# Kernel tuning notes

Measured on AMD Instinct MI355X. Metric: run time of the kernel, lower is better.

## Reference

```python
import jax, jax.numpy as jnp
import numpy as np

PATCH = 16  # patch_size

def _patchify(images, p=PATCH):
    # images: [B, H, W] -> patches: [B, N, p*p] in raster order
    B, H, W = images.shape
    x = images.reshape(B, H // p, p, W // p, p)
    x = x.transpose(0, 1, 3, 2, 4)  # [B, H/p, W/p, p, p]
    return x.reshape(B, (H // p) * (W // p), p * p)

def setup_inputs() -> dict:
    key = jax.random.key(0)
    k1, k2 = jax.random.split(key)
    images = jax.random.normal(k1, (64, 256, 256), dtype=jnp.float32)
    vocab = jax.random.normal(k2, (4096, 256), dtype=jnp.float32)  # [V, patch^2]
    return {"images": images, "vocab": vocab}

def reference(images, vocab):
    # forward_patches: patchify (raster ordering -> identity permutation)
    patches = _patchify(images)  # [B, N, D]
    # forward_tokens: torch.cdist + argmin. argmin of Euclidean distance
    # equals argmin of squared distance; expand ||x-v||^2 to avoid the
    # explicit [B, N, V, D] difference tensor.
    v2 = jnp.sum(vocab * vocab, axis=-1)                      # [V]
    xv = jnp.einsum('bnd,vd->bnv', patches, vocab)            # [B, N, V]
    x2 = jnp.sum(patches * patches, axis=-1, keepdims=True)   # [B, N, 1]
    d2 = x2 - 2.0 * xv + v2                                   # [B, N, V]
    tokens = jnp.argmin(d2, axis=-1)                          # [B, N] int
    return patches, tokens
```

## Files before the change

### kernel.cpp

```cpp
#include <hip/hip_runtime.h>
#include <math.h>

#define PS      16
#define D       256
#define V       4096
#define M       16384
#define NSPLIT  64
#define PAIR_CAP 1048576
#define QMARGIN 130

typedef _Float16 half8 __attribute__((ext_vector_type(8)));
typedef _Float16 half4 __attribute__((ext_vector_type(4)));
typedef float    f32x4 __attribute__((ext_vector_type(4)));

__device__ __forceinline__ void gload_lds16(const void* g, void* l) {
  __builtin_amdgcn_global_load_lds(
      (const __attribute__((address_space(1))) unsigned int*)g,
      (__attribute__((address_space(3))) unsigned int*)l, 16, 0, 0);
}


__global__ __launch_bounds__(256) void prep_kernel(
    const float* __restrict__ img, const float* __restrict__ vocab,
    float* __restrict__ outp, _Float16* __restrict__ Ah2,
    _Float16* __restrict__ Vh2, float* __restrict__ v2,
    int* __restrict__ paircount) {
  if (blockIdx.x < 4096) {
    if (blockIdx.x == 0 && threadIdx.x == 0) *paircount = 0;
    const int t  = blockIdx.x * 256 + threadIdx.x;
    const int o4 = t << 2;
    const int m   = o4 >> 8;
    const int d   = o4 & 255;
    const int b   = m >> 8;
    const int n   = m & 255;
    const int py = n >> 4, px = n & 15, i = d >> 4, j = d & 15;
    const float4 v = *(const float4*)(img + (b << 16) + ((py * PS + i) << 8) + px * PS + j);
    *(float4*)(outp + o4) = v;
    half4 h = { (_Float16)v.x, (_Float16)v.y, (_Float16)v.z, (_Float16)v.w };
    const int fa = (m >> 6) * 16384 + (d >> 5) * 2048 + ((m >> 4) & 3) * 512 +
                   ((d >> 3) & 3) * 128 + (m & 15) * 8 + (d & 7);
    *(half4*)(Ah2 + fa) = h;
  } else {
    const int gtid = (blockIdx.x - 4096) * 256 + threadIdx.x;
    const int c    = gtid >> 6;
    const int lane = gtid & 63;
    const int d0   = lane << 2;
    const float4 v = *(const float4*)(vocab + (size_t)c * D + d0);
    half4 h = { (_Float16)v.x, (_Float16)v.y, (_Float16)v.z, (_Float16)v.w };
    const int fv = (c >> 8) * 65536 + (d0 >> 5) * 8192 + ((c >> 4) & 15) * 512 +
                   ((d0 >> 3) & 3) * 128 + (c & 15) * 8 + (d0 & 7);
    *(half4*)(Vh2 + fv) = h;
    float s = v.x * v.x + v.y * v.y + v.z * v.z + v.w * v.w;
    #pragma unroll
    for (int off = 32; off > 0; off >>= 1) s += __shfl_down(s, off);
    if (lane == 0) v2[c] = s;
  }
}

__global__ __launch_bounds__(512, 6) void gemm_score_kernel(
    const _Float16* __restrict__ Ah2,
    const _Float16* __restrict__ Vh2,
    const float* __restrict__ v2,
    unsigned* __restrict__ pk1, unsigned* __restrict__ pk2) {
  __shared__ __align__(16) _Float16 Af[8 * 64 * 32];

  const int tid  = threadIdx.x;
  const int lane = tid & 63;
  const int wid  = tid >> 6;
  const int sp     = blockIdx.x;
  const int rowblk = blockIdx.y;
  const int row0 = rowblk * 64;
  const int c0w  = sp * 256 + wid * 32;

  {
    const _Float16* src = Ah2 + (size_t)rowblk * 16384 + wid * 2048 + lane * 8;
    _Float16* dst = Af + wid * 2048;
    #pragma unroll
    for (int t = 0; t < 4; ++t)
      gload_lds16(src + t * 512, dst + t * 512);
  }
  __syncthreads();

  const int cl = lane & 15;
  const int q  = lane >> 4;
  const _Float16* Ak = Af + q * 128 + cl * 8;
  const _Float16* Bk = Vh2 + sp * 65536 + wid * 1024 +
                       q * 128 + cl * 8;

  f32x4 acc[2][4];
  #pragma unroll
  for (int i = 0; i < 2; ++i)
    #pragma unroll
    for (int j = 0; j < 4; ++j) acc[i][j] = (f32x4){0.f, 0.f, 0.f, 0.f};

  half8 av0[2], av1[2], bp[4];
#define LAV(B, OFF) do {                                            \
    B[0] = *(const half8*)(Bk + (OFF));                             \
    B[1] = *(const half8*)(Bk + (OFF) + 512);                       \
  } while (0)
#define LBP(OFF) do {                                               \
    bp[0] = *(const half8*)(Ak + (OFF));                            \
    bp[1] = *(const half8*)(Ak + (OFF) + 512);                      \
    bp[2] = *(const half8*)(Ak + (OFF) + 1024);                     \
    bp[3] = *(const half8*)(Ak + (OFF) + 1536);                     \
  } while (0)
#define MMC(AV) do {                                                \
    __builtin_amdgcn_s_setprio(1);                                  \
    acc[0][0] = __builtin_amdgcn_mfma_f32_16x16x32_f16(AV[0], bp[0], acc[0][0], 0, 0, 0); \
    acc[0][1] = __builtin_amdgcn_mfma_f32_16x16x32_f16(AV[0], bp[1], acc[0][1], 0, 0, 0); \
    acc[0][2] = __builtin_amdgcn_mfma_f32_16x16x32_f16(AV[0], bp[2], acc[0][2], 0, 0, 0); \
    acc[0][3] = __builtin_amdgcn_mfma_f32_16x16x32_f16(AV[0], bp[3], acc[0][3], 0, 0, 0); \
    acc[1][0] = __builtin_amdgcn_mfma_f32_16x16x32_f16(AV[1], bp[0], acc[1][0], 0, 0, 0); \
    acc[1][1] = __builtin_amdgcn_mfma_f32_16x16x32_f16(AV[1], bp[1], acc[1][1], 0, 0, 0); \
    acc[1][2] = __builtin_amdgcn_mfma_f32_16x16x32_f16(AV[1], bp[2], acc[1][2], 0, 0, 0); \
    acc[1][3] = __builtin_amdgcn_mfma_f32_16x16x32_f16(AV[1], bp[3], acc[1][3], 0, 0, 0); \
    __builtin_amdgcn_s_setprio(0);                                  \
  } while (0)

  LAV(av0, 0);
  #pragma unroll 1
  for (int kt2 = 0; kt2 < 3; ++kt2) {
    LAV(av1, 8192);
    LBP(0);
    MMC(av0);
    LAV(av0, 16384);
    LBP(2048);
    MMC(av1);
    Bk += 16384; Ak += 4096;
  }
  LAV(av1, 8192);
  LBP(0);
  MMC(av0);
  LBP(2048);
  MMC(av1);
#undef LAV
#undef LBP
#undef MMC

  float Cv[8];
  #pragma unroll
  for (int i = 0; i < 2; ++i) {
    const float4 vq = *(const float4*)(v2 + c0w + i * 16 + q * 4);
    #pragma unroll
    for (int r = 0; r < 4; ++r) Cv[i * 4 + r] = fmaf(vq[r], 512.0f, 524288.0f);
  }
  unsigned wk1[4], wk2[4];
  #pragma unroll
  for (int j = 0; j < 4; ++j) {
    unsigned K1 = 0xFFFFFFFFu, K2 = 0xFFFFFFFFu;
    #pragma unroll
    for (int i = 0; i < 2; ++i)
      #pragma unroll
      for (int r = 0; r < 4; ++r) {
        const unsigned key =
            ((unsigned)fmaf(-1024.0f, acc[i][j][r], Cv[i * 4 + r]) << 12) |
            (unsigned)(c0w + i * 16 + q * 4 + r);
        K2 = min(K2, max(K1, key));
        K1 = min(K1, key);
      }
    #pragma unroll
    for (int mask = 16; mask <= 32; mask <<= 1) {
      const unsigned o1 = (unsigned)__shfl_xor((int)K1, mask);
      const unsigned o2 = (unsigned)__shfl_xor((int)K2, mask);
      K2 = min(min(K2, o2), max(K1, o1));
      K1 = min(K1, o1);
    }
    wk1[j] = K1; wk2[j] = K2;
  }
  __syncthreads();
  unsigned* scr = (unsigned*)Af;
  if (q == 0) {
    #pragma unroll
    for (int j = 0; j < 4; ++j) {
      const int idx = (wid >> 1) * 256 + (wid & 1) * 128 + (j * 16 + cl) * 2;
      scr[idx] = wk1[j]; scr[idx + 1] = wk2[j];
    }
  }
  __syncthreads();
  if (tid < 256) {
    const int pair = tid >> 6, row = tid & 63;
    const unsigned a1k = scr[pair * 256 + row * 2], a2k = scr[pair * 256 + row * 2 + 1];
    const unsigned b1k = scr[pair * 256 + 128 + row * 2], b2k = scr[pair * 256 + 128 + row * 2 + 1];
    const unsigned K2 = min(min(a2k, b2k), max(a1k, b1k));
    const unsigned K1 = min(a1k, b1k);
    const int grp = sp * 4 + pair;
    pk1[(size_t)grp * M + row0 + row] = K1;
    pk2[(size_t)grp * M + row0 + row] = K2;
  }
}

__global__ __launch_bounds__(256) void reduce_gather_kernel(
    const unsigned* __restrict__ pk1, const unsigned* __restrict__ pk2,
    float* __restrict__ tok, unsigned long long* __restrict__ minkey,
    unsigned* __restrict__ pairs, int* __restrict__ paircount) {
  __shared__ unsigned r1[4][64], r2[4][64];
  const int tid = threadIdx.x;
  const int mo  = tid & 63;
  const int wid = tid >> 6;
  const int m = blockIdx.x * 64 + mo;
  unsigned K1 = 0xFFFFFFFFu, K2 = 0xFFFFFFFFu;
  for (int s = wid * 16; s < wid * 16 + 16; ++s) {
    const unsigned b1 = pk1[(size_t)s * M + m];
    const unsigned b2 = pk2[(size_t)s * M + m];
    K2 = min(min(K2, b2), max(K1, b1));
    K1 = min(K1, b1);
  }
  r1[wid][mo] = K1; r2[wid][mo] = K2;
  __syncthreads();
  if (tid < 64) {
    K1 = 0xFFFFFFFFu; K2 = 0xFFFFFFFFu;
    #pragma unroll
    for (int w = 0; w < 4; ++w) {
      const unsigned b1 = r1[w][mo], b2 = r2[w][mo];
      K2 = min(min(K2, b2), max(K1, b1));
      K1 = min(K1, b1);
    }
    tok[m] = (float)(K1 & 4095u);
    minkey[m] = 0xFFFFFFFFFFFFFFFFull;
    if ((int)(K2 >> 12) - (int)(K1 >> 12) <= QMARGIN) {
      const int th = (int)(K1 >> 12) + QMARGIN;
      int cnt = 0;
      for (int s = 0; s < NSPLIT; ++s) {
        const unsigned b1 = pk1[(size_t)s * M + m];
        const unsigned b2 = pk2[(size_t)s * M + m];
        cnt += ((int)(b2 >> 12) <= th) ? 64
             : (((int)(b1 >> 12) <= th) ? 1 : 0);
      }
      int base = atomicAdd(paircount, cnt);
      if (base + cnt <= PAIR_CAP) {
        const unsigned mh = (unsigned)m << 12;
        for (int s = 0; s < NSPLIT; ++s) {
          const unsigned b1 = pk1[(size_t)s * M + m];
          const unsigned b2 = pk2[(size_t)s * M + m];
          if ((int)(b2 >> 12) <= th) {
            for (int r = 0; r < 64; ++r) pairs[base + r] = mh | (unsigned)(s * 64 + r);
            base += 64;
          } else if ((int)(b1 >> 12) <= th) {
            pairs[base++] = mh | (b1 & 4095u);
          }
        }
      }
    }
  }
}

__global__ __launch_bounds__(256) void refine_score(
    const float* __restrict__ patches, const float* __restrict__ vocab,
    const unsigned* __restrict__ pairs, const int* __restrict__ paircount,
    unsigned long long* __restrict__ minkey) {
  const int lane = threadIdx.x & 63;
  const int gw = (blockIdx.x * 256 + threadIdx.x) >> 6;
  const int nw = (gridDim.x * 256) >> 6;
  int np = *paircount;
  if (np > PAIR_CAP) np = PAIR_CAP;
  for (int i = gw; i < np; i += nw) {
    const unsigned pr = pairs[i];
    const int m = pr >> 12, row = pr & 4095;
    const float4 pv = *(const float4*)(patches + (size_t)m * D + (lane << 2));
    const float4 vv = *(const float4*)(vocab + (size_t)row * D + (lane << 2));
    double acc = 0.0, df;
    df = (double)pv.x - (double)vv.x; acc = fma(df, df, acc);
    df = (double)pv.y - (double)vv.y; acc = fma(df, df, acc);
    df = (double)pv.z - (double)vv.z; acc = fma(df, df, acc);
    df = (double)pv.w - (double)vv.w; acc = fma(df, df, acc);
    #pragma unroll
    for (int off = 32; off > 0; off >>= 1) acc += __shfl_down(acc, off);
    if (lane == 0) {
      const unsigned long long key =
          ((unsigned long long)__double_as_longlong(acc) & ~0xFFFull) | (unsigned)row;
      atomicMin(&minkey[m], key);
    }
  }
}

__global__ __launch_bounds__(256) void refine_final(
    const unsigned* __restrict__ pairs, const int* __restrict__ paircount,
    const unsigned long long* __restrict__ minkey, float* __restrict__ tok) {
  int np = *paircount;
  if (np > PAIR_CAP) np = PAIR_CAP;
  for (int i = blockIdx.x * 256 + threadIdx.x; i < np; i += gridDim.x * 256) {
    const int m = pairs[i] >> 12;
    tok[m] = (float)(unsigned)(minkey[m] & 4095ull);
  }
}

extern "C" void kernel_launch(void* const* d_in, const int* in_sizes, int n_in,
                              void* d_out, int out_size, void* d_ws, size_t ws_size,
                              hipStream_t stream) {
  const float* images = (const float*)d_in[0];
  const float* vocab  = (const float*)d_in[1];
  float* out     = (float*)d_out;
  float* patches = out;
  float* tokens  = out + (size_t)M * D;

  char* ws = (char*)d_ws;
  _Float16* Ah2      = (_Float16*)(ws);
  _Float16* Vh2      = (_Float16*)(ws + 8388608);
  float*    v2       = (float*)   (ws + 10485760);
  unsigned* pk1      = (unsigned*)(ws + 10502144);
  unsigned* pk2      = (unsigned*)(ws + 14696448);
  unsigned long long* minkey = (unsigned long long*)(ws + 18890752);
  int*      paircount= (int*)     (ws + 19021824);
  unsigned* pairs    = (unsigned*)(ws + 19021888);

  prep_kernel<<<4096 + 1024, 256, 0, stream>>>(images, vocab, patches, Ah2,
                                               Vh2, v2, paircount);
  gemm_score_kernel<<<dim3(V / 256, M / 64), 512, 0, stream>>>(Ah2, Vh2, v2, pk1, pk2);
  reduce_gather_kernel<<<M / 64, 256, 0, stream>>>(pk1, pk2, tokens, minkey,
                                                   pairs, paircount);
  refine_score<<<512, 256, 0, stream>>>(patches, vocab, pairs, paircount, minkey);
  refine_final<<<64, 256, 0, stream>>>(pairs, paircount, minkey, tokens);
}
```

Baseline: 151.0 us.

## Switch GEMM to 32x32x16 MFMA with matching fragment layouts

Replaces the 16x16x32 MFMA tiling with 32x32x16 MFMA instructions, issuing four larger MFMAs per step instead of eight. The prep kernel writes A and V fp16 in new fragment-friendly layouts to match. The epilogue top-2 reduction is reworked for the new accumulator layout, which needs one cross-half shuffle instead of two. The refine_score grid is also enlarged from 512 to 2048 blocks. The larger MFMA is meant to raise matrix-core throughput and cut per-tile instruction overhead, at the cost of layout changes that must stay consistent across kernels.

```diff
diff --git a/kernel.cpp b/kernel.cpp
--- a/kernel.cpp
+++ b/kernel.cpp
@@ -11,7 +11,7 @@
 
 typedef _Float16 half8 __attribute__((ext_vector_type(8)));
 typedef _Float16 half4 __attribute__((ext_vector_type(4)));
-typedef float    f32x4 __attribute__((ext_vector_type(4)));
+typedef float    f32x16 __attribute__((ext_vector_type(16)));
 
 __device__ __forceinline__ void gload_lds16(const void* g, void* l) {
   __builtin_amdgcn_global_load_lds(
@@ -37,8 +37,8 @@
     const float4 v = *(const float4*)(img + (b << 16) + ((py * PS + i) << 8) + px * PS + j);
     *(float4*)(outp + o4) = v;
     half4 h = { (_Float16)v.x, (_Float16)v.y, (_Float16)v.z, (_Float16)v.w };
-    const int fa = (m >> 6) * 16384 + (d >> 5) * 2048 + ((m >> 4) & 3) * 512 +
-                   ((d >> 3) & 3) * 128 + (m & 15) * 8 + (d & 7);
+    const int fa = (m >> 6) * 16384 + (d >> 4) * 1024 + ((m >> 5) & 1) * 512 +
+                   ((m & 31) + ((d >> 3) & 1) * 32) * 8 + (d & 7);
     *(half4*)(Ah2 + fa) = h;
   } else {
     const int gtid = (blockIdx.x - 4096) * 256 + threadIdx.x;
@@ -47,8 +47,8 @@
     const int d0   = lane << 2;
     const float4 v = *(const float4*)(vocab + (size_t)c * D + d0);
     half4 h = { (_Float16)v.x, (_Float16)v.y, (_Float16)v.z, (_Float16)v.w };
-    const int fv = (c >> 8) * 65536 + (d0 >> 5) * 8192 + ((c >> 4) & 15) * 512 +
-                   ((d0 >> 3) & 3) * 128 + (c & 15) * 8 + (d0 & 7);
+    const int fv = (c >> 5) * 8192 + (d0 >> 4) * 512 +
+                   ((c & 31) + ((d0 >> 3) & 1) * 32) * 8 + (d0 & 7);
     *(half4*)(Vh2 + fv) = h;
     float s = v.x * v.x + v.y * v.y + v.z * v.z + v.w * v.w;
     #pragma unroll
@@ -81,17 +81,14 @@
   }
   __syncthreads();
 
-  const int cl = lane & 15;
-  const int q  = lane >> 4;
-  const _Float16* Ak = Af + q * 128 + cl * 8;
-  const _Float16* Bk = Vh2 + sp * 65536 + wid * 1024 +
-                       q * 128 + cl * 8;
-
-  f32x4 acc[2][4];
+  const _Float16* Ak = Af + lane * 8;
+  const _Float16* Bk = Vh2 + (sp * 8 + wid) * 8192 + lane * 8;
+
+  f32x16 acc[2];
   #pragma unroll
-  for (int i = 0; i < 2; ++i)
-    #pragma unroll
-    for (int j = 0; j < 4; ++j) acc[i][j] = (f32x4){0.f, 0.f, 0.f, 0.f};
+  for (int j = 0; j < 2; ++j)
+    #pragma unroll
+    for (int r = 0; r < 16; ++r) acc[j][r] = 0.f;
 
   half8 av0[2], av1[2], bp[4];
 #define LAV(B, OFF) do {                                            \
@@ -106,29 +103,25 @@
   } while (0)
 #define MMC(AV) do {                                                \
     __builtin_amdgcn_s_setprio(1);                                  \
-    acc[0][0] = __builtin_amdgcn_mfma_f32_16x16x32_f16(AV[0], bp[0], acc[0][0], 0, 0, 0); \
-    acc[0][1] = __builtin_amdgcn_mfma_f32_16x16x32_f16(AV[0], bp[1], acc[0][1], 0, 0, 0); \
-    acc[0][2] = __builtin_amdgcn_mfma_f32_16x16x32_f16(AV[0], bp[2], acc[0][2], 0, 0, 0); \
-    acc[0][3] = __builtin_amdgcn_mfma_f32_16x16x32_f16(AV[0], bp[3], acc[0][3], 0, 0, 0); \
-    acc[1][0] = __builtin_amdgcn_mfma_f32_16x16x32_f16(AV[1], bp[0], acc[1][0], 0, 0, 0); \
-    acc[1][1] = __builtin_amdgcn_mfma_f32_16x16x32_f16(AV[1], bp[1], acc[1][1], 0, 0, 0); \
-    acc[1][2] = __builtin_amdgcn_mfma_f32_16x16x32_f16(AV[1], bp[2], acc[1][2], 0, 0, 0); \
-    acc[1][3] = __builtin_amdgcn_mfma_f32_16x16x32_f16(AV[1], bp[3], acc[1][3], 0, 0, 0); \
+    acc[0] = __builtin_amdgcn_mfma_f32_32x32x16_f16(AV[0], bp[0], acc[0], 0, 0, 0); \
+    acc[1] = __builtin_amdgcn_mfma_f32_32x32x16_f16(AV[0], bp[1], acc[1], 0, 0, 0); \
+    acc[0] = __builtin_amdgcn_mfma_f32_32x32x16_f16(AV[1], bp[2], acc[0], 0, 0, 0); \
+    acc[1] = __builtin_amdgcn_mfma_f32_32x32x16_f16(AV[1], bp[3], acc[1], 0, 0, 0); \
     __builtin_amdgcn_s_setprio(0);                                  \
   } while (0)
 
   LAV(av0, 0);
   #pragma unroll 1
   for (int kt2 = 0; kt2 < 3; ++kt2) {
-    LAV(av1, 8192);
+    LAV(av1, 1024);
     LBP(0);
     MMC(av0);
-    LAV(av0, 16384);
+    LAV(av0, 2048);
     LBP(2048);
     MMC(av1);
-    Bk += 16384; Ak += 4096;
-  }
-  LAV(av1, 8192);
+    Bk += 2048; Ak += 4096;
+  }
+  LAV(av1, 1024);
   LBP(0);
   MMC(av0);
   LBP(2048);
@@ -137,50 +130,48 @@
 #undef LBP
 #undef MMC
 
-  float Cv[8];
+  const int h  = lane >> 5;
+  const int pc = lane & 31;
+  float Cv[16];
   #pragma unroll
-  for (int i = 0; i < 2; ++i) {
-    const float4 vq = *(const float4*)(v2 + c0w + i * 16 + q * 4);
-    #pragma unroll
-    for (int r = 0; r < 4; ++r) Cv[i * 4 + r] = fmaf(vq[r], 512.0f, 524288.0f);
-  }
-  unsigned wk1[4], wk2[4];
+  for (int b = 0; b < 4; ++b) {
+    const float4 vq = *(const float4*)(v2 + c0w + 4 * h + b * 8);
+    #pragma unroll
+    for (int e = 0; e < 4; ++e) Cv[b * 4 + e] = fmaf(vq[e], 512.0f, 524288.0f);
+  }
+  unsigned wk1[2], wk2[2];
   #pragma unroll
-  for (int j = 0; j < 4; ++j) {
+  for (int j = 0; j < 2; ++j) {
     unsigned K1 = 0xFFFFFFFFu, K2 = 0xFFFFFFFFu;
     #pragma unroll
-    for (int i = 0; i < 2; ++i)
-      #pragma unroll
-      for (int r = 0; r < 4; ++r) {
-        const unsigned key =
-            ((unsigned)fmaf(-1024.0f, acc[i][j][r], Cv[i * 4 + r]) << 12) |
-            (unsigned)(c0w + i * 16 + q * 4 + r);
-        K2 = min(K2, max(K1, key));
-        K1 = min(K1, key);
-      }
-    #pragma unroll
-    for (int mask = 16; mask <= 32; mask <<= 1) {
-      const unsigned o1 = (unsigned)__shfl_xor((int)K1, mask);
-      const unsigned o2 = (unsigned)__shfl_xor((int)K2, mask);
-      K2 = min(min(K2, o2), max(K1, o1));
-      K1 = min(K1, o1);
-    }
+    for (int r = 0; r < 16; ++r) {
+      const unsigned key =
+          ((unsigned)fmaf(-1024.0f, acc[j][r], Cv[r]) << 12) |
+          (unsigned)(c0w + (r & 3) + 8 * (r >> 2) + 4 * h);
+      K2 = min(K2, max(K1, key));
+      K1 = min(K1, key);
+    }
+    const unsigned o1 = (unsigned)__shfl_xor((int)K1, 32);
+    const unsigned o2 = (unsigned)__shfl_xor((int)K2, 32);
+    K2 = min(min(K2, o2), max(K1, o1));
+    K1 = min(K1, o1);
     wk1[j] = K1; wk2[j] = K2;
   }
   __syncthreads();
-  unsigned* scr = (unsigned*)Af;
-  if (q == 0) {
-    #pragma unroll
-    for (int j = 0; j < 4; ++j) {
-      const int idx = (wid >> 1) * 256 + (wid & 1) * 128 + (j * 16 + cl) * 2;
-      scr[idx] = wk1[j]; scr[idx + 1] = wk2[j];
+  unsigned* scr1 = (unsigned*)Af;
+  unsigned* scr2 = scr1 + 512;
+  if (h == 0) {
+    #pragma unroll
+    for (int j = 0; j < 2; ++j) {
+      const int idx = wid * 64 + j * 32 + pc;
+      scr1[idx] = wk1[j]; scr2[idx] = wk2[j];
     }
   }
   __syncthreads();
   if (tid < 256) {
     const int pair = tid >> 6, row = tid & 63;
-    const unsigned a1k = scr[pair * 256 + row * 2], a2k = scr[pair * 256 + row * 2 + 1];
-    const unsigned b1k = scr[pair * 256 + 128 + row * 2], b2k = scr[pair * 256 + 128 + row * 2 + 1];
+    const unsigned a1k = scr1[(pair * 2) * 64 + row], a2k = scr2[(pair * 2) * 64 + row];
+    const unsigned b1k = scr1[(pair * 2 + 1) * 64 + row], b2k = scr2[(pair * 2 + 1) * 64 + row];
     const unsigned K2 = min(min(a2k, b2k), max(a1k, b1k));
     const unsigned K1 = min(a1k, b1k);
     const int grp = sp * 4 + pair;
@@ -308,6 +299,6 @@
   gemm_score_kernel<<<dim3(V / 256, M / 64), 512, 0, stream>>>(Ah2, Vh2, v2, pk1, pk2);
   reduce_gather_kernel<<<M / 64, 256, 0, stream>>>(pk1, pk2, tokens, minkey,
                                                    pairs, paircount);
-  refine_score<<<512, 256, 0, stream>>>(patches, vocab, pairs, paircount, minkey);
+  refine_score<<<2048, 256, 0, stream>>>(patches, vocab, pairs, paircount, minkey);
   refine_final<<<64, 256, 0, stream>>>(pairs, paircount, minkey, tokens);
 }
```

Result: slower. 158.3 us (+4.9%).
